# Optimization experiments

Hardware: AMD Instinct MI355X
Metric: run time of the kernel (lower is better)

## Reference

```python
import jax, jax.numpy as jnp
import numpy as np

B, T, C, U = 256, 1024, 128, 100   # batch, time, num_classes (incl. blank), max label len
BLANK = C - 1                      # TF/Keras CTC: blank is the LAST class
NEG = -1.0e30                      # log-space -inf surrogate (fp32-safe)
EPS = 1e-7                         # keras backend epsilon used in ctc_batch_cost


def setup_inputs() -> dict:
    key = jax.random.key(0)
    k1, k2, k3 = jax.random.split(key, 3)
    # ctc_batch_cost consumes post-softmax probabilities
    logits = jax.random.normal(k1, (B, T, C), dtype=jnp.float32)
    y_pred = jax.nn.softmax(logits, axis=-1)
    y_true = jax.random.randint(k2, (B, U), 0, BLANK)          # labels in [0, C-2]
    label_len = jax.random.randint(k3, (B,), 1, U + 1)         # 1..U
    return {"y_pred": y_pred, "y_true": y_true, "label_len": label_len}


def _ctc_batch_cost(y_pred, y_true, label_len):
    # log probs, matching keras: log(prob + epsilon)
    logp = jnp.log(y_pred + EPS)                               # [B,T,C]
    S = 2 * U + 1
    # extended label sequence: blank, l1, blank, l2, ..., blank
    ext = jnp.full((B, S), BLANK, dtype=y_true.dtype)
    ext = ext.at[:, 1::2].set(y_true)                          # [B,S]
    # skip (s-2 -> s) allowed iff ext[s] != blank and ext[s] != ext[s-2]
    can_skip = jnp.concatenate(
        [jnp.zeros((B, 2), dtype=bool),
         (ext[:, 2:] != BLANK) & (ext[:, 2:] != ext[:, :-2])], axis=1)  # [B,S]

    logp_t = jnp.transpose(logp, (1, 0, 2))                    # [T,B,C]
    # t = 0 init: only s=0 (blank) and s=1 (first label) reachable
    lp0 = jnp.take_along_axis(logp_t[0], ext, axis=1)          # [B,S]
    alpha0 = jnp.full((B, S), NEG, dtype=logp.dtype)
    alpha0 = alpha0.at[:, 0].set(lp0[:, 0]).at[:, 1].set(lp0[:, 1])

    def step(alpha, lp_c):
        # lp_c: [B,C] log probs at time t; gather per extended-label position
        lp = jnp.take_along_axis(lp_c, ext, axis=1)            # [B,S]
        a1 = jnp.pad(alpha[:, :-1], ((0, 0), (1, 0)), constant_values=NEG)
        a2 = jnp.pad(alpha[:, :-2], ((0, 0), (2, 0)), constant_values=NEG)
        a2 = jnp.where(can_skip, a2, NEG)
        alpha = jax.nn.logsumexp(jnp.stack([alpha, a1, a2]), axis=0) + lp
        return alpha, None

    alpha, _ = jax.lax.scan(step, alpha0, logp_t[1:])          # [B,S]
    # total log-likelihood ends at s = 2L-1 (last label) or s = 2L (trailing blank)
    end = 2 * label_len[:, None]                               # [B,1]
    a_end = jnp.take_along_axis(alpha, jnp.concatenate([end - 1, end], axis=1), axis=1)
    return -jax.nn.logsumexp(a_end, axis=1, keepdims=True)     # [B,1] per-example loss


def reference(y_pred, y_true, label_len):
    # matches tf.keras.backend.ctc_batch_cost(y_true, y_pred, fill(T), label_len)
    return _ctc_batch_cost(y_pred, y_true, label_len)
```

## Files before the change

### kernel.cpp

```cpp
#include <hip/hip_runtime.h>


#define Bc 256
#define Tc 1024
#define Cc 128
#define Uc 100
#define BLANKc 127
#define EPSc 1e-7f
#define LN2f 0.69314718055994530942f
#define RSTRIDE 130
#define NSLOT 128
#define QD 8

__global__ __launch_bounds__(64) void ctc_skew_kernel(
    const float* __restrict__ y_pred,
    const int*   __restrict__ y_true,
    const int*   __restrict__ label_len,
    float*       __restrict__ out)
{
    __shared__ float rowbuf[NSLOT * RSTRIDE];
    __shared__ float shA[204];
    __shared__ int   shE[64];

    const int b    = blockIdx.x;
    const int lane = threadIdx.x;
    const float* gp = y_pred + (size_t)b * (Tc * Cc);

    const int k0  = 2*lane, k1 = 2*lane+1;
    const int k0c = k0 < Uc ? k0 : Uc-1;
    const int k1c = k1 < Uc ? k1 : Uc-1;
    const int y0  = y_true[b*Uc + k0c];
    const int y1  = y_true[b*Uc + k1c];
    int ym1 = y0;
    if (lane > 0) ym1 = y_true[b*Uc + k0 - 1];
    const float ms1 = (lane > 0 && y0 != ym1) ? 1.0f : 0.0f;
    const float ms3 = (y1 != y0) ? 1.0f : 0.0f;
    const float mh  = (lane > 0) ? 1.0f : 0.0f;

    float a0=0.f, a1=0.f, a2=0.f, a3=0.f;
    if (lane == 0) { a0 = gp[BLANKc]+EPSc; a1 = gp[y0]+EPSc; }
    int e = 0;

#pragma unroll
    for (int i = 0; i < 8; ++i) {
        const int f4  = i*64 + lane;
        const int row = f4 >> 5;
        const int c4  = (f4 & 31) * 4;
        const float4 v = *(const float4*)(gp + row*Cc + c4);
        float* dst = &rowbuf[row*RSTRIDE + c4];
        dst[0]=v.x; dst[1]=v.y; dst[2]=v.z; dst[3]=v.w;
    }

    float2 Q[QD];
#pragma unroll
    for (int k = 0; k < QD; ++k)
        Q[k] = *(const float2*)(gp + (16+k)*Cc + lane*2);

    float q2a = 0.f, q1a = 0.f;
    int   q2e = 0,   q1e = 0;

    auto body = [&](int n, int j, bool fzp) {
        const int rr = n - lane;
        const int rc = (rr < 0 ? 0 : rr) & (NSLOT-1);
        const float* rowp = &rowbuf[rc * RSTRIDE];
        const float pbr = rowp[BLANKc];
        const float p0r = rowp[y0];
        const float p1r = rowp[y1];
        const int j8 = (n-1) & (QD-1);
        const int ws = (n+15) & (NSLOT-1);
        *(float2*)&rowbuf[ws*RSTRIDE + lane*2] = Q[j8];
        int lr = n+23; lr = lr > Tc-1 ? Tc-1 : lr;
        Q[j8] = *(const float2*)(gp + lr*Cc + lane*2);
        const float h1r = q2a; const int el = q2e;
        q2a = q1a; q2e = q1e;
        int d = el - e; d = d > 126 ? 126 : d;
        const float h1 = mh * ldexpf(h1r, d);
        const float pb = pbr + EPSc, p0 = p0r + EPSc, p1 = p1r + EPSc;
        const float n0 = (a0 + h1) * pb;
        const float n1 = (a1 + a0 + ms1*h1) * p0;
        const float n2 = (a2 + a1) * pb;
        const float n3 = (a3 + a2 + ms3*a1) * p1;
        const float sm = (n0+n1)+(n2+n3);
        const int   en = (sm > 0.0f) ? e : el;
        bool upd = true;
        if (fzp) upd = (lane >= n - (Tc-1));
        if (upd) { a0=n0; a1=n1; a2=n2; a3=n3; e=en; }
        if ((j & 3) == 3) {
            const float m = fmaxf(fmaxf(a0,a1), fmaxf(a2,a3));
            int ex = (int)((__float_as_uint(m) >> 23) & 0xFF) - 127;
            ex = (m > 0.0f) ? ex : 0;
            a0 = ldexpf(a0,-ex); a1 = ldexpf(a1,-ex);
            a2 = ldexpf(a2,-ex); a3 = ldexpf(a3,-ex);
            e += ex;
        }
        q1a = __shfl_up(a3, 1, 64);
        q1e = __shfl_up(e , 1, 64);
    };

    int n = 1;
    for (int c = 0; c < 63; ++c) {
#pragma unroll
        for (int j = 0; j < 16; ++j) { body(n, j, false); ++n; }
    }
    for (int c = 0; c < 4; ++c) {
#pragma unroll
        for (int j = 0; j < 16; ++j) { body(n, j, true); ++n; }
    }
#pragma unroll
    for (int j = 0; j < 14; ++j) { body(n, j, true); ++n; }

    if (lane < 51) {
        shA[4*lane+0] = a0; shA[4*lane+1] = a1;
        shA[4*lane+2] = a2; shA[4*lane+3] = a3;
        shE[lane] = e;
    }
    __syncthreads();
    if (lane == 0) {
        const int L  = label_len[b];
        const int s1 = 2*L - 1, s2 = 2*L;
        const float v1 = shA[s1], v2 = shA[s2];
        const int   e1 = shE[s1 >> 2], e2 = shE[s2 >> 2];
        const int   em = e1 > e2 ? e1 : e2;
        const float sum = ldexpf(v1, e1-em) + ldexpf(v2, e2-em);
        const float r   = __log2f(sum) + (float)em;
        out[b] = -LN2f * r;
    }
}

extern "C" void kernel_launch(void* const* d_in, const int* in_sizes, int n_in,
                              void* d_out, int out_size, void* d_ws, size_t ws_size,
                              hipStream_t stream) {
    const float* y_pred    = (const float*)d_in[0];
    const int*   y_true    = (const int*)d_in[1];
    const int*   label_len = (const int*)d_in[2];
    float*       out       = (float*)d_out;
    ctc_skew_kernel<<<Bc, 64, 0, stream>>>(y_pred, y_true, label_len, out);
}
```

Baseline: 266.9 us.

## Skew wavefront by four steps per lane and prefetch emission probs into registers

Changes the anti-diagonal skew so each lane lags its neighbour by four time steps instead of one. This gives the inter-lane shuffle dependency a multi-step slack and lets the exponent exchange happen once per four steps. Emission probabilities are prefetched PF steps ahead into register queues, and blank probabilities go into a separate compact LDS array written by lane 63. The ring buffer doubles to 256 rows and the total step count grows to cover the longer skew. The trade is more total serial steps and extra LDS, in exchange for hiding shuffle and LDS latency on the critical recurrence.

```diff
diff --git a/kernel.cpp b/kernel.cpp
--- a/kernel.cpp
+++ b/kernel.cpp
@@ -9,8 +9,10 @@
 #define EPSc 1e-7f
 #define LN2f 0.69314718055994530942f
 #define RSTRIDE 130
-#define NSLOT 128
+#define NSLOT 256
 #define QD 8
+#define PF 8
+#define NTOT 1223
 
 __global__ __launch_bounds__(64) void ctc_skew_kernel(
     const float* __restrict__ y_pred,
@@ -19,11 +21,13 @@
     float*       __restrict__ out)
 {
     __shared__ float rowbuf[NSLOT * RSTRIDE];
+    __shared__ float blkbuf[NSLOT];
     __shared__ float shA[204];
     __shared__ int   shE[64];
 
-    const int b    = blockIdx.x;
-    const int lane = threadIdx.x;
+    const int b     = blockIdx.x;
+    const int lane  = threadIdx.x;
+    const int lane4 = lane * 4;
     const float* gp = y_pred + (size_t)b * (Tc * Cc);
 
     const int k0  = 2*lane, k1 = 2*lane+1;
@@ -50,51 +54,76 @@
         float* dst = &rowbuf[row*RSTRIDE + c4];
         dst[0]=v.x; dst[1]=v.y; dst[2]=v.z; dst[3]=v.w;
     }
+    if (lane < 16)
+        blkbuf[((lane & 3) << 6) | ((lane >> 2) & 63)] =
+            rowbuf[lane*RSTRIDE + BLANKc];
 
     float2 Q[QD];
 #pragma unroll
     for (int k = 0; k < QD; ++k)
         Q[k] = *(const float2*)(gp + (16+k)*Cc + lane*2);
 
-    float q2a = 0.f, q1a = 0.f;
-    int   q2e = 0,   q1e = 0;
+    float PQb[PF], PQ0[PF], PQ1[PF];
+#pragma unroll
+    for (int k = 0; k < PF; ++k) {
+        int rr = (k+1) - lane4; rr = rr < 0 ? 0 : rr;
+        const float* rp = &rowbuf[(rr & (NSLOT-1)) * RSTRIDE];
+        PQ0[k] = rp[y0]; PQ1[k] = rp[y1];
+        PQb[k] = blkbuf[((rr & 3) << 6) | ((rr >> 2) & 63)];
+    }
+
+    float HQ[8] = {0,0,0,0,0,0,0,0};
+    int   ER[2] = {0,0};
+    float hscale = mh;
+    int   el_blk = 0;
+    int   rbase  = PF - lane4;
 
     auto body = [&](int n, int j, bool fzp) {
-        const int rr = n - lane;
-        const int rc = (rr < 0 ? 0 : rr) & (NSLOT-1);
-        const float* rowp = &rowbuf[rc * RSTRIDE];
-        const float pbr = rowp[BLANKc];
-        const float p0r = rowp[y0];
-        const float p1r = rowp[y1];
-        const int j8 = (n-1) & (QD-1);
-        const int ws = (n+15) & (NSLOT-1);
-        *(float2*)&rowbuf[ws*RSTRIDE + lane*2] = Q[j8];
-        int lr = n+23; lr = lr > Tc-1 ? Tc-1 : lr;
-        Q[j8] = *(const float2*)(gp + lr*Cc + lane*2);
-        const float h1r = q2a; const int el = q2e;
-        q2a = q1a; q2e = q1e;
-        int d = el - e; d = d > 126 ? 126 : d;
-        const float h1 = mh * ldexpf(h1r, d);
-        const float pb = pbr + EPSc, p0 = p0r + EPSc, p1 = p1r + EPSc;
+        const int qi = j & 7;
+        if ((j & 3) == 0) {
+            el_blk = ER[(j >> 2) & 1];
+            int d = el_blk - e; d = d > 126 ? 126 : d;
+            hscale = ldexpf(mh, d);
+        }
+        const float pb = PQb[qi] + EPSc;
+        const float p0 = PQ0[qi] + EPSc;
+        const float p1 = PQ1[qi] + EPSc;
+        rbase += 1;
+        int rcl = rbase; rcl = rcl < 0 ? 0 : rcl; rcl = rcl > Tc-1 ? Tc-1 : rcl;
+        {
+            const float* rp = &rowbuf[(rcl & (NSLOT-1)) * RSTRIDE];
+            PQ0[qi] = rp[y0];
+            PQ1[qi] = rp[y1];
+            PQb[qi] = blkbuf[((rcl & 3) << 6) | ((rcl >> 2) & 63)];
+        }
+        {
+            const int ws = (n + 15) & (NSLOT-1);
+            *(float2*)&rowbuf[ws * RSTRIDE + lane*2] = Q[qi];
+            if (lane == 63) {
+                const int wb = n + 15;
+                blkbuf[((wb & 3) << 6) | ((wb >> 2) & 63)] = Q[qi].y;
+            }
+            int lr = n + 23; lr = lr > Tc-1 ? Tc-1 : lr;
+            Q[qi] = *(const float2*)(gp + lr*Cc + lane*2);
+        }
+        const float h1 = HQ[(j + 3) & 7] * hscale;
         const float n0 = (a0 + h1) * pb;
         const float n1 = (a1 + a0 + ms1*h1) * p0;
         const float n2 = (a2 + a1) * pb;
         const float n3 = (a3 + a2 + ms3*a1) * p1;
-        const float sm = (n0+n1)+(n2+n3);
-        const int   en = (sm > 0.0f) ? e : el;
         bool upd = true;
-        if (fzp) upd = (lane >= n - (Tc-1));
-        if (upd) { a0=n0; a1=n1; a2=n2; a3=n3; e=en; }
+        if (fzp) upd = (lane4 >= n - (Tc-1));
+        if (upd) { a0=n0; a1=n1; a2=n2; a3=n3; }
         if ((j & 3) == 3) {
             const float m = fmaxf(fmaxf(a0,a1), fmaxf(a2,a3));
             int ex = (int)((__float_as_uint(m) >> 23) & 0xFF) - 127;
-            ex = (m > 0.0f) ? ex : 0;
+            ex = (m > 0.0f) ? ex : (el_blk - e);
             a0 = ldexpf(a0,-ex); a1 = ldexpf(a1,-ex);
             a2 = ldexpf(a2,-ex); a3 = ldexpf(a3,-ex);
             e += ex;
         }
-        q1a = __shfl_up(a3, 1, 64);
-        q1e = __shfl_up(e , 1, 64);
+        HQ[j & 7] = __shfl_up(a3, 1, 64);
+        if ((j & 3) == 3) ER[(j >> 2) & 1] = __shfl_up(e, 1, 64);
     };
 
     int n = 1;
@@ -102,12 +131,12 @@
 #pragma unroll
         for (int j = 0; j < 16; ++j) { body(n, j, false); ++n; }
     }
-    for (int c = 0; c < 4; ++c) {
+    for (int c = 0; c < 13; ++c) {
 #pragma unroll
         for (int j = 0; j < 16; ++j) { body(n, j, true); ++n; }
     }
 #pragma unroll
-    for (int j = 0; j < 14; ++j) { body(n, j, true); ++n; }
+    for (int j = 0; j < 7; ++j) { body(n, j, true); ++n; }
 
     if (lane < 51) {
         shA[4*lane+0] = a0; shA[4*lane+1] = a1;
```

Result: slower. 278.6 us (+4.4%).

## Split CTC wavefront across two waves with LDS halo ring

Applied to the files above, without the earlier changes.

Splits the 201 extended-label states across two 64-lane waves. Each lane now holds 2 states instead of 4, and the second wave trails the first by a few chunks, reading boundary alphas through an LDS halo ring. This is meant to shorten the per-step serial dependency chain and roughly halve the work per lane. In exchange it adds a block barrier every 16 steps, a larger LDS row buffer and the pipeline skew of the second wave.

```diff
diff --git a/kernel.cpp b/kernel.cpp
--- a/kernel.cpp
+++ b/kernel.cpp
@@ -9,41 +9,35 @@
 #define EPSc 1e-7f
 #define LN2f 0.69314718055994530942f
 #define RSTRIDE 130
-#define NSLOT 128
+#define NSLOT 192
+#define SLOTW (NSLOT*RSTRIDE)
 #define QD 8
-
-__global__ __launch_bounds__(64) void ctc_skew_kernel(
+#define HRING 128
+#define NCHUNK 72
+
+__global__ __launch_bounds__(128) void ctc_dual_kernel(
     const float* __restrict__ y_pred,
     const int*   __restrict__ y_true,
     const int*   __restrict__ label_len,
     float*       __restrict__ out)
 {
-    __shared__ float rowbuf[NSLOT * RSTRIDE];
-    __shared__ float shA[204];
-    __shared__ int   shE[64];
-
+    __shared__ float  rowbuf[SLOTW];
+    __shared__ float2 hal[HRING];
+    __shared__ float  shA[204];
+    __shared__ int    shE[128];
+
+    const int tid  = threadIdx.x;
+    const int wid  = tid >> 6;
+    const int lane = tid & 63;
     const int b    = blockIdx.x;
-    const int lane = threadIdx.x;
     const float* gp = y_pred + (size_t)b * (Tc * Cc);
 
-    const int k0  = 2*lane, k1 = 2*lane+1;
-    const int k0c = k0 < Uc ? k0 : Uc-1;
-    const int k1c = k1 < Uc ? k1 : Uc-1;
-    const int y0  = y_true[b*Uc + k0c];
-    const int y1  = y_true[b*Uc + k1c];
-    int ym1 = y0;
-    if (lane > 0) ym1 = y_true[b*Uc + k0 - 1];
-    const float ms1 = (lane > 0 && y0 != ym1) ? 1.0f : 0.0f;
-    const float ms3 = (y1 != y0) ? 1.0f : 0.0f;
-    const float mh  = (lane > 0) ? 1.0f : 0.0f;
-
-    float a0=0.f, a1=0.f, a2=0.f, a3=0.f;
-    if (lane == 0) { a0 = gp[BLANKc]+EPSc; a1 = gp[y0]+EPSc; }
-    int e = 0;
-
-#pragma unroll
-    for (int i = 0; i < 8; ++i) {
-        const int f4  = i*64 + lane;
+    for (int i = 0; i < SLOTW/128; ++i) rowbuf[i*128 + tid] = 0.f;
+    if (tid < HRING) hal[tid] = make_float2(0.f, __int_as_float(0));
+
+#pragma unroll
+    for (int i = 0; i < 4; ++i) {
+        const int f4  = i*128 + tid;
         const int row = f4 >> 5;
         const int c4  = (f4 & 31) * 4;
         const float4 v = *(const float4*)(gp + row*Cc + c4);
@@ -51,79 +45,150 @@
         dst[0]=v.x; dst[1]=v.y; dst[2]=v.z; dst[3]=v.w;
     }
 
+    int yme; float ms, mh;
+    if (wid == 0) {
+        yme = y_true[b*Uc + lane];
+        const int yl = (lane > 0) ? y_true[b*Uc + lane - 1] : yme;
+        ms = (lane > 0 && yme != yl) ? 1.0f : 0.0f;
+        mh = (lane > 0) ? 1.0f : 0.0f;
+    } else {
+        const int li = 37 + lane;
+        yme = y_true[b*Uc + (li > Uc-1 ? Uc-1 : li)];
+        const int yl = y_true[b*Uc + (li - 1 > Uc-1 ? Uc-1 : li - 1)];
+        ms = (yme != yl) ? 1.0f : 0.0f;
+        mh = 1.0f;
+    }
+
+    float a0 = 0.f, a1 = 0.f; int e = 0;
+    if (wid == 0 && lane == 0) { a0 = gp[BLANKc]+EPSc; a1 = gp[yme]+EPSc; }
+
+    int sw = ((1 - lane + NSLOT) % NSLOT) * RSTRIDE - RSTRIDE;
+    if (sw < 0) sw += SLOTW;
+
     float2 Q[QD];
-#pragma unroll
-    for (int k = 0; k < QD; ++k)
-        Q[k] = *(const float2*)(gp + (16+k)*Cc + lane*2);
-
-    float q2a = 0.f, q1a = 0.f;
-    int   q2e = 0,   q1e = 0;
-
-    auto body = [&](int n, int j, bool fzp) {
-        const int rr = n - lane;
-        const int rc = (rr < 0 ? 0 : rr) & (NSLOT-1);
-        const float* rowp = &rowbuf[rc * RSTRIDE];
-        const float pbr = rowp[BLANKc];
-        const float p0r = rowp[y0];
-        const float p1r = rowp[y1];
-        const int j8 = (n-1) & (QD-1);
-        const int ws = (n+15) & (NSLOT-1);
-        *(float2*)&rowbuf[ws*RSTRIDE + lane*2] = Q[j8];
-        int lr = n+23; lr = lr > Tc-1 ? Tc-1 : lr;
-        Q[j8] = *(const float2*)(gp + lr*Cc + lane*2);
+    int wslot = 16 * RSTRIDE;
+    if (wid == 0) {
+#pragma unroll
+        for (int k = 0; k < QD; ++k)
+            Q[k] = *(const float2*)(gp + (16+k)*Cc + lane*2);
+    }
+    __syncthreads();
+
+    float q2a = 0.f, q1a = 0.f; int q2e = 0, q1e = 0;
+    float r2a = 0.f, r1a = 0.f; int r2e = 0, r1e = 0;
+
+    auto lstep = [&](int n, int j, bool fzp) {
+        sw += RSTRIDE; if (sw >= SLOTW) sw -= SLOTW;
+        const float pbr = rowbuf[sw + BLANKc];
+        const float p0r = rowbuf[sw + yme];
+        const int qi = (n-1) & (QD-1);
+        *(float2*)&rowbuf[wslot + lane*2] = Q[qi];
+        wslot += RSTRIDE; if (wslot >= SLOTW) wslot -= SLOTW;
+        int lr = n + 23; lr = lr > Tc-1 ? Tc-1 : lr;
+        Q[qi] = *(const float2*)(gp + lr*Cc + lane*2);
         const float h1r = q2a; const int el = q2e;
         q2a = q1a; q2e = q1e;
         int d = el - e; d = d > 126 ? 126 : d;
         const float h1 = mh * ldexpf(h1r, d);
-        const float pb = pbr + EPSc, p0 = p0r + EPSc, p1 = p1r + EPSc;
+        const float pb = pbr + EPSc, p0 = p0r + EPSc;
         const float n0 = (a0 + h1) * pb;
-        const float n1 = (a1 + a0 + ms1*h1) * p0;
-        const float n2 = (a2 + a1) * pb;
-        const float n3 = (a3 + a2 + ms3*a1) * p1;
-        const float sm = (n0+n1)+(n2+n3);
+        const float n1 = (a1 + a0 + ms*h1) * p0;
+        const float sm = n0 + n1;
         const int   en = (sm > 0.0f) ? e : el;
         bool upd = true;
         if (fzp) upd = (lane >= n - (Tc-1));
-        if (upd) { a0=n0; a1=n1; a2=n2; a3=n3; e=en; }
+        if (upd) { a0 = n0; a1 = n1; e = en; }
         if ((j & 3) == 3) {
-            const float m = fmaxf(fmaxf(a0,a1), fmaxf(a2,a3));
+            const float m = fmaxf(a0, a1);
             int ex = (int)((__float_as_uint(m) >> 23) & 0xFF) - 127;
             ex = (m > 0.0f) ? ex : 0;
-            a0 = ldexpf(a0,-ex); a1 = ldexpf(a1,-ex);
-            a2 = ldexpf(a2,-ex); a3 = ldexpf(a3,-ex);
+            a0 = ldexpf(a0, -ex); a1 = ldexpf(a1, -ex);
             e += ex;
         }
-        q1a = __shfl_up(a3, 1, 64);
+        if (lane == 36) hal[n & (HRING-1)] = make_float2(a1, __int_as_float(e));
+        q1a = __shfl_up(a1, 1, 64);
         q1e = __shfl_up(e , 1, 64);
     };
 
-    int n = 1;
-    for (int c = 0; c < 63; ++c) {
-#pragma unroll
-        for (int j = 0; j < 16; ++j) { body(n, j, false); ++n; }
-    }
-    for (int c = 0; c < 4; ++c) {
-#pragma unroll
-        for (int j = 0; j < 16; ++j) { body(n, j, true); ++n; }
-    }
-#pragma unroll
-    for (int j = 0; j < 14; ++j) { body(n, j, true); ++n; }
-
-    if (lane < 51) {
-        shA[4*lane+0] = a0; shA[4*lane+1] = a1;
-        shA[4*lane+2] = a2; shA[4*lane+3] = a3;
-        shE[lane] = e;
+    auto tstep = [&](int m, int j, bool fzp) {
+        sw += RSTRIDE; if (sw >= SLOTW) sw -= SLOTW;
+        const float pbr = rowbuf[sw + BLANKc];
+        const float p0r = rowbuf[sw + yme];
+        const float h1r = (lane == 0) ? r2a : q2a;
+        const int   el  = (lane == 0) ? r2e : q2e;
+        q2a = q1a; q2e = q1e;
+        r2a = r1a; r2e = r1e;
+        {
+            const float2 hv = hal[(m + 37) & (HRING-1)];
+            r1a = hv.x; r1e = __float_as_int(hv.y);
+        }
+        int d = el - e; d = d > 126 ? 126 : d;
+        const float h1 = ldexpf(h1r, d);
+        const float pb = pbr + EPSc, p0 = p0r + EPSc;
+        const float n0 = (a0 + h1) * pb;
+        const float n1 = (a1 + a0 + ms*h1) * p0;
+        const float sm = n0 + n1;
+        const int   en = (sm > 0.0f) ? e : el;
+        bool upd = true;
+        if (fzp) upd = (lane >= m - (Tc-1));
+        if (upd) { a0 = n0; a1 = n1; e = en; }
+        if ((j & 3) == 3) {
+            const float mx = fmaxf(a0, a1);
+            int ex = (int)((__float_as_uint(mx) >> 23) & 0xFF) - 127;
+            ex = (mx > 0.0f) ? ex : 0;
+            a0 = ldexpf(a0, -ex); a1 = ldexpf(a1, -ex);
+            e += ex;
+        }
+        q1a = __shfl_up(a1, 1, 64);
+        q1e = __shfl_up(e , 1, 64);
+    };
+
+    int n = 1, m = 1;
+    for (int c = 0; c < NCHUNK; ++c) {
+        if (wid == 0) {
+            if (c >= 63) {
+#pragma unroll
+                for (int j = 0; j < 16; ++j) { lstep(n, j, true);  ++n; }
+            } else {
+#pragma unroll
+                for (int j = 0; j < 16; ++j) { lstep(n, j, false); ++n; }
+            }
+        } else if (c >= 4) {
+            if (c == 4) {
+                float2 h2 = hal[36], h1v = hal[37];
+                r2a = h2.x;  r2e = __float_as_int(h2.y);
+                r1a = h1v.x; r1e = __float_as_int(h1v.y);
+            }
+            if (c >= 67) {
+#pragma unroll
+                for (int j = 0; j < 16; ++j) { tstep(m, j, true);  ++m; }
+            } else {
+#pragma unroll
+                for (int j = 0; j < 16; ++j) { tstep(m, j, false); ++m; }
+            }
+        }
+        __syncthreads();
+    }
+
+    if (wid == 0) {
+        if (lane <= 36) {
+            shA[2*lane]   = a0; shA[2*lane+1] = a1;
+            shE[lane]     = e;
+        }
+    } else {
+        shA[74 + 2*lane] = a0; shA[75 + 2*lane] = a1;
+        shE[64 + lane]   = e;
     }
     __syncthreads();
-    if (lane == 0) {
+    if (tid == 0) {
         const int L  = label_len[b];
         const int s1 = 2*L - 1, s2 = 2*L;
         const float v1 = shA[s1], v2 = shA[s2];
-        const int   e1 = shE[s1 >> 2], e2 = shE[s2 >> 2];
-        const int   em = e1 > e2 ? e1 : e2;
+        const int e1 = shE[s1 < 74 ? (s1 >> 1) : 64 + ((s1 - 74) >> 1)];
+        const int e2 = shE[s2 < 74 ? (s2 >> 1) : 64 + ((s2 - 74) >> 1)];
+        const int em = e1 > e2 ? e1 : e2;
         const float sum = ldexpf(v1, e1-em) + ldexpf(v2, e2-em);
-        const float r   = __log2f(sum) + (float)em;
-        out[b] = -LN2f * r;
+        out[b] = -LN2f * (__log2f(sum) + (float)em);
     }
 }
 
@@ -134,5 +199,5 @@
     const int*   y_true    = (const int*)d_in[1];
     const int*   label_len = (const int*)d_in[2];
     float*       out       = (float*)d_out;
-    ctc_skew_kernel<<<Bc, 64, 0, stream>>>(y_pred, y_true, label_len, out);
+    ctc_dual_kernel<<<Bc, 128, 0, stream>>>(y_pred, y_true, label_len, out);
 }
```

Measured after the change: 624.7 us. +134.0%, slower.

## Cut per-step overhead in skewed CTC recurrence: exponent shuffles, addressing, epsilon, tail

Applied to the files above, without the earlier changes.

The epsilon is now added once when rows are written to shared memory, rather than on every read. Slot addresses advance as byte offsets. The exponent is shuffled between lanes only at renormalization steps (every 4th) instead of every step, with exponents double-buffered in ELa/ELb. The shared row buffer is zero-initialized so early clamped reads behave, and the final tail is cut to a single step because only lanes below 51 contribute to the output. This shortens the serial per-step critical path, at the cost of subtler exponent bookkeeping whose correctness depends on the renormalization schedule.

```diff
diff --git a/kernel.cpp b/kernel.cpp
--- a/kernel.cpp
+++ b/kernel.cpp
@@ -10,6 +10,7 @@
 #define LN2f 0.69314718055994530942f
 #define RSTRIDE 130
 #define NSLOT 128
+#define SLOTB (NSLOT*RSTRIDE*4)
 #define QD 8
 
 __global__ __launch_bounds__(64) void ctc_skew_kernel(
@@ -18,13 +19,14 @@
     const int*   __restrict__ label_len,
     float*       __restrict__ out)
 {
-    __shared__ float rowbuf[NSLOT * RSTRIDE];
+    __shared__ __align__(16) float rowbuf[NSLOT * RSTRIDE];
     __shared__ float shA[204];
     __shared__ int   shE[64];
 
     const int b    = blockIdx.x;
     const int lane = threadIdx.x;
     const float* gp = y_pred + (size_t)b * (Tc * Cc);
+    char* rb = (char*)rowbuf;
 
     const int k0  = 2*lane, k1 = 2*lane+1;
     const int k0c = k0 < Uc ? k0 : Uc-1;
@@ -36,19 +38,27 @@
     const float ms1 = (lane > 0 && y0 != ym1) ? 1.0f : 0.0f;
     const float ms3 = (y1 != y0) ? 1.0f : 0.0f;
     const float mh  = (lane > 0) ? 1.0f : 0.0f;
+    const int y0b = y0 * 4, y1b = y1 * 4;
 
     float a0=0.f, a1=0.f, a2=0.f, a3=0.f;
     if (lane == 0) { a0 = gp[BLANKc]+EPSc; a1 = gp[y0]+EPSc; }
     int e = 0;
+
+    {
+        const float4 z = make_float4(0.f, 0.f, 0.f, 0.f);
+        float4* rb4 = (float4*)rowbuf;
+#pragma unroll
+        for (int i = 0; i < 65; ++i) rb4[i*64 + lane] = z;
+    }
 
 #pragma unroll
     for (int i = 0; i < 8; ++i) {
         const int f4  = i*64 + lane;
         const int row = f4 >> 5;
         const int c4  = (f4 & 31) * 4;
-        const float4 v = *(const float4*)(gp + row*Cc + c4);
+        float4 v = *(const float4*)(gp + row*Cc + c4);
         float* dst = &rowbuf[row*RSTRIDE + c4];
-        dst[0]=v.x; dst[1]=v.y; dst[2]=v.z; dst[3]=v.w;
+        dst[0]=v.x+EPSc; dst[1]=v.y+EPSc; dst[2]=v.z+EPSc; dst[3]=v.w+EPSc;
     }
 
     float2 Q[QD];
@@ -56,45 +66,49 @@
     for (int k = 0; k < QD; ++k)
         Q[k] = *(const float2*)(gp + (16+k)*Cc + lane*2);
 
+    int swb = (((1 - lane) & (NSLOT-1)) * RSTRIDE - RSTRIDE) * 4;
+    if (swb < 0) swb += SLOTB;
+    int wswb = 15 * RSTRIDE * 4;
+    const int lane8 = lane * 8;
+
     float q2a = 0.f, q1a = 0.f;
-    int   q2e = 0,   q1e = 0;
+    int ELa = 0, ELb = 0;
 
     auto body = [&](int n, int j, bool fzp) {
-        const int rr = n - lane;
-        const int rc = (rr < 0 ? 0 : rr) & (NSLOT-1);
-        const float* rowp = &rowbuf[rc * RSTRIDE];
-        const float pbr = rowp[BLANKc];
-        const float p0r = rowp[y0];
-        const float p1r = rowp[y1];
-        const int j8 = (n-1) & (QD-1);
-        const int ws = (n+15) & (NSLOT-1);
-        *(float2*)&rowbuf[ws*RSTRIDE + lane*2] = Q[j8];
-        int lr = n+23; lr = lr > Tc-1 ? Tc-1 : lr;
-        Q[j8] = *(const float2*)(gp + lr*Cc + lane*2);
-        const float h1r = q2a; const int el = q2e;
-        q2a = q1a; q2e = q1e;
+        swb += RSTRIDE*4; if (swb >= SLOTB) swb -= SLOTB;
+        const float pb = *(const float*)(rb + swb + BLANKc*4);
+        const float p0 = *(const float*)(rb + swb + y0b);
+        const float p1 = *(const float*)(rb + swb + y1b);
+        wswb += RSTRIDE*4; if (wswb >= SLOTB) wswb -= SLOTB;
+        float2 qv = Q[j & 7];
+        qv.x += EPSc; qv.y += EPSc;
+        *(float2*)(rb + wswb + lane8) = qv;
+        int lr = n + 23; lr = lr > Tc-1 ? Tc-1 : lr;
+        Q[j & 7] = *(const float2*)(gp + lr*Cc + lane*2);
+        const int el = ((j == 0) || (j >= 5 && j <= 8) || (j >= 13)) ? ELb : ELa;
+        const float h1r = q2a; q2a = q1a;
         int d = el - e; d = d > 126 ? 126 : d;
         const float h1 = mh * ldexpf(h1r, d);
-        const float pb = pbr + EPSc, p0 = p0r + EPSc, p1 = p1r + EPSc;
         const float n0 = (a0 + h1) * pb;
         const float n1 = (a1 + a0 + ms1*h1) * p0;
         const float n2 = (a2 + a1) * pb;
         const float n3 = (a3 + a2 + ms3*a1) * p1;
-        const float sm = (n0+n1)+(n2+n3);
-        const int   en = (sm > 0.0f) ? e : el;
         bool upd = true;
         if (fzp) upd = (lane >= n - (Tc-1));
-        if (upd) { a0=n0; a1=n1; a2=n2; a3=n3; e=en; }
+        if (upd) { a0=n0; a1=n1; a2=n2; a3=n3; }
         if ((j & 3) == 3) {
             const float m = fmaxf(fmaxf(a0,a1), fmaxf(a2,a3));
             int ex = (int)((__float_as_uint(m) >> 23) & 0xFF) - 127;
-            ex = (m > 0.0f) ? ex : 0;
+            ex = (m > 0.0f) ? ex : (el - e);
             a0 = ldexpf(a0,-ex); a1 = ldexpf(a1,-ex);
             a2 = ldexpf(a2,-ex); a3 = ldexpf(a3,-ex);
             e += ex;
         }
         q1a = __shfl_up(a3, 1, 64);
-        q1e = __shfl_up(e , 1, 64);
+        if ((j & 3) == 3) {
+            const int es = __shfl_up(e, 1, 64);
+            if (j == 3 || j == 11) ELb = es; else ELa = es;
+        }
     };
 
     int n = 1;
@@ -106,8 +120,7 @@
 #pragma unroll
         for (int j = 0; j < 16; ++j) { body(n, j, true); ++n; }
     }
-#pragma unroll
-    for (int j = 0; j < 14; ++j) { body(n, j, true); ++n; }
+    body(n, 0, true);
 
     if (lane < 51) {
         shA[4*lane+0] = a0; shA[4*lane+1] = a1;
```

Result: faster. 252.0 us (-5.6%).
